# Performance work log

Hardware: AMD Instinct MI355X
Metric: run time of the kernel (lower is better)

## Reference

```python
import jax, jax.numpy as jnp
import numpy as np


def setup_inputs() -> dict:
    key = jax.random.key(0)
    k1, k2, k3, k4, k5 = jax.random.split(key, 5)
    N, V, C = 4096, 4, 256
    desc = jax.random.normal(k1, (N, V, C), dtype=jnp.float32)
    sf = jax.random.normal(k2, (N, V, C), dtype=jnp.float32)
    T = jax.random.normal(k3, (V, 4, 4), dtype=jnp.float32)
    W_rec = jax.random.normal(k4, (C, C), dtype=jnp.float32) * (1.0 / np.sqrt(C))
    W_T = jax.random.normal(k5, (32, C), dtype=jnp.float32) * (1.0 / np.sqrt(32))
    return {"desc": desc, "sf": sf, "T": T, "W_rec": W_rec, "W_T": W_T}


def reference(desc, sf, T, W_rec, W_T):
    # desc, sf: [N, V, C]; T: [V, 4, 4]
    N, V, C = desc.shape
    # F.normalize(desc, dim=2)
    dn = desc / jnp.maximum(jnp.linalg.norm(desc, axis=2, keepdims=True), 1e-12)
    ar = jnp.arange(N)
    loss_total = jnp.zeros((), dtype=desc.dtype)
    count = jnp.zeros((), dtype=desc.dtype)
    for i in range(V):
        for j in range(V):
            if i == j:
                continue
            di = dn[:, i, :]  # [N, C]
            dj = dn[:, j, :]  # [N, C]
            sim = di @ dj.T   # [N, N]
            idx_ij = jnp.argmax(sim, axis=1)
            idx_ji = jnp.argmax(sim, axis=0)
            mutual = (idx_ji[idx_ij] == ar)  # [N] bool, mutual nearest neighbors
            # kpnet.reconstruction(desc_i, T_i, T_j): linear, transform-conditioned
            rel = jnp.concatenate([T[i].ravel(), T[j].ravel()])  # [32]
            sf_recon = di @ W_rec + rel @ W_T  # [N, C]
            # torch.no_grad() block -> stop_gradient
            prob = jax.nn.softmax(sim, axis=1)
            sf_j_soft = jax.lax.stop_gradient(prob @ sf[:, j, :])  # [N, C]
            m = mutual.astype(desc.dtype)[:, None]  # [N, 1]
            n_sel = jnp.sum(m)
            sq = jnp.sum(((sf_recon - sf_j_soft) ** 2) * m)
            pair_loss = sq / jnp.maximum(n_sel * C, 1.0)  # masked MSE (mean over selected elems)
            valid = (n_sel > 0).astype(desc.dtype)
            loss_total = loss_total + valid * pair_loss
            count = count + valid
    return jnp.where(count > 0, loss_total / jnp.maximum(count, 1.0), 0.0 * jnp.sum(desc))
```

## Files before the change

kernel.cpp:

```cpp
#include <hip/hip_runtime.h>
#include <math.h>

#define N_ 4096
#define V_ 4
#define C_ 256

typedef __attribute__((ext_vector_type(8))) short bf16x8;
typedef __attribute__((ext_vector_type(4))) float f32x4;
typedef unsigned long long u64;

#define OFF_R      0ull
#define OFF_DNHI   16777216ull
#define OFF_DNLO   25165824ull
#define OFF_SFT    33554432ull
#define OFF_E      37748736ull
#define OFF_ET     88080384ull
#define OFF_WTH    138412032ull
#define OFF_WTL    138543104ull
#define OFF_ROWPK  138674176ull
#define OFF_COLPK  138870784ull
#define OFF_ROWSM  139067392ull
#define OFF_COLSM  139165696ull
#define OFF_RELWT  139264000ull
#define OFF_SQ     139280384ull
#define OFF_CNT    139280448ull

__device__ __forceinline__ unsigned short f2bf(float x) {
    unsigned int u = __float_as_uint(x);
    u += 0x7fffu + ((u >> 16) & 1u);
    return (unsigned short)(u >> 16);
}
__device__ __forceinline__ float bf2f(unsigned short h) {
    return __uint_as_float(((unsigned int)h) << 16);
}
__device__ __forceinline__ f32x4 mfma16(bf16x8 a, bf16x8 b, f32x4 c) {
    return __builtin_amdgcn_mfma_f32_16x16x32_bf16(a, b, c, 0, 0, 0);
}
__device__ __forceinline__ unsigned int pk4fp8(float x0, float x1, float x2, float x3) {
    int w = 0;
    w = __builtin_amdgcn_cvt_pk_fp8_f32(x0, x1, w, false);
    w = __builtin_amdgcn_cvt_pk_fp8_f32(x2, x3, w, true);
    return (unsigned int)w;
}

__global__ void normalize_k(const float* __restrict__ desc,
                            unsigned short* __restrict__ dnh, unsigned short* __restrict__ dnl) {
    int row = blockIdx.x;
    int n = row >> 2, v = row & 3;
    int c = threadIdx.x;
    float x = desc[(size_t)row * C_ + c];
    __shared__ float red[256];
    red[c] = x * x;
    __syncthreads();
    for (int s = 128; s > 0; s >>= 1) {
        if (c < s) red[c] += red[c + s];
        __syncthreads();
    }
    float inv = 1.0f / fmaxf(sqrtf(red[0]), 1e-12f);
    float y = x * inv;
    size_t o = ((size_t)v * N_ + n) * C_ + c;
    unsigned short h = f2bf(y);
    dnh[o] = h;
    dnl[o] = f2bf(y - bf2f(h));
}

__global__ void wrecT_k(const float* __restrict__ W, unsigned short* __restrict__ WTh,
                        unsigned short* __restrict__ WTl) {
    __shared__ float Tt[64 * 65];
    int k0 = blockIdx.x * 64, c0 = blockIdx.y * 64;
    int t = threadIdx.x;
    int kr = t >> 2, cq = (t & 3) * 16;
    const float* src = W + (size_t)(k0 + kr) * C_ + c0 + cq;
    for (int u = 0; u < 16; ++u) Tt[(cq + u) * 65 + kr] = src[u];
    __syncthreads();
    int cr = t >> 2, kq = (t & 3) * 16;
    unsigned short th[16] __attribute__((aligned(16)));
    unsigned short tl[16] __attribute__((aligned(16)));
    for (int u = 0; u < 16; ++u) {
        float x = Tt[cr * 65 + kq + u];
        unsigned short h = f2bf(x);
        th[u] = h; tl[u] = f2bf(x - bf2f(h));
    }
    size_t o = (size_t)(c0 + cr) * C_ + k0 + kq;
    *(uint4*)(WTh + o) = *(const uint4*)th;
    *(uint4*)(WTh + o + 8) = *(const uint4*)(th + 8);
    *(uint4*)(WTl + o) = *(const uint4*)tl;
    *(uint4*)(WTl + o + 8) = *(const uint4*)(tl + 8);
}

__global__ __launch_bounds__(256) void rmatmul_k(
    const unsigned short* __restrict__ Ah, const unsigned short* __restrict__ Al,
    const unsigned short* __restrict__ Bh, const unsigned short* __restrict__ Bl,
    float* __restrict__ R) {
    __shared__ unsigned short smem[4 * 128 * 40];
    unsigned short* sAh = smem;
    unsigned short* sAl = sAh + 128 * 40;
    unsigned short* sBh = sAl + 128 * 40;
    unsigned short* sBl = sBh + 128 * 40;
    int tid = threadIdx.x;
    int c0 = blockIdx.x * 128, m0 = blockIdx.y * 128;
    int w = tid >> 6, l = tid & 63, wm = w & 1, wn = w >> 1;
    int mr = l & 15, q = l >> 4;
    f32x4 acc[4][4];
#pragma unroll
    for (int a = 0; a < 4; ++a)
#pragma unroll
        for (int b = 0; b < 4; ++b)
#pragma unroll
            for (int u = 0; u < 4; ++u) acc[a][b][u] = 0.f;
    int r = tid >> 1, h = (tid & 1) * 16;
    for (int k0 = 0; k0 < C_; k0 += 32) {
        size_t ga = (size_t)(m0 + r) * C_ + k0 + h;
        size_t gb = (size_t)(c0 + r) * C_ + k0 + h;
        uint4 a0 = *(const uint4*)(Ah + ga);
        uint4 a1 = *(const uint4*)(Ah + ga + 8);
        uint4 a2 = *(const uint4*)(Al + ga);
        uint4 a3 = *(const uint4*)(Al + ga + 8);
        uint4 b0 = *(const uint4*)(Bh + gb);
        uint4 b1 = *(const uint4*)(Bh + gb + 8);
        uint4 b2 = *(const uint4*)(Bl + gb);
        uint4 b3 = *(const uint4*)(Bl + gb + 8);
        *(uint4*)(sAh + r * 40 + h)     = a0;
        *(uint4*)(sAh + r * 40 + h + 8) = a1;
        *(uint4*)(sAl + r * 40 + h)     = a2;
        *(uint4*)(sAl + r * 40 + h + 8) = a3;
        *(uint4*)(sBh + r * 40 + h)     = b0;
        *(uint4*)(sBh + r * 40 + h + 8) = b1;
        *(uint4*)(sBl + r * 40 + h)     = b2;
        *(uint4*)(sBl + r * 40 + h + 8) = b3;
        __syncthreads();
        bf16x8 fah[4], fal[4], fbh[4], fbl[4];
#pragma unroll
        for (int ti = 0; ti < 4; ++ti) {
            int row = wm * 64 + ti * 16 + mr;
            fah[ti] = *(const bf16x8*)(sAh + row * 40 + q * 8);
            fal[ti] = *(const bf16x8*)(sAl + row * 40 + q * 8);
        }
#pragma unroll
        for (int tj = 0; tj < 4; ++tj) {
            int row = wn * 64 + tj * 16 + mr;
            fbh[tj] = *(const bf16x8*)(sBh + row * 40 + q * 8);
            fbl[tj] = *(const bf16x8*)(sBl + row * 40 + q * 8);
        }
#pragma unroll
        for (int ti = 0; ti < 4; ++ti)
#pragma unroll
            for (int tj = 0; tj < 4; ++tj) acc[ti][tj] = mfma16(fah[ti], fbh[tj], acc[ti][tj]);
#pragma unroll
        for (int ti = 0; ti < 4; ++ti)
#pragma unroll
            for (int tj = 0; tj < 4; ++tj) acc[ti][tj] = mfma16(fah[ti], fbl[tj], acc[ti][tj]);
#pragma unroll
        for (int ti = 0; ti < 4; ++ti)
#pragma unroll
            for (int tj = 0; tj < 4; ++tj) acc[ti][tj] = mfma16(fal[ti], fbh[tj], acc[ti][tj]);
        __syncthreads();
    }
#pragma unroll
    for (int ti = 0; ti < 4; ++ti)
#pragma unroll
        for (int tj = 0; tj < 4; ++tj) {
            int c = c0 + wn * 64 + tj * 16 + mr;
#pragma unroll
            for (int rg = 0; rg < 4; ++rg) {
                int m = m0 + wm * 64 + ti * 16 + q * 4 + rg;
                R[(size_t)m * C_ + c] = acc[ti][tj][rg];
            }
        }
}

__global__ void relwt_k(const float* __restrict__ T, const float* __restrict__ WT,
                        float* __restrict__ relwt) {
    int p = blockIdx.x; int i = p >> 2, j = p & 3;
    if (i == j) return;
    int c = threadIdx.x;
    float acc = 0.f;
    for (int k = 0; k < 16; ++k) acc += T[i * 16 + k] * WT[(size_t)k * C_ + c];
    for (int k = 0; k < 16; ++k) acc += T[j * 16 + k] * WT[(size_t)(16 + k) * C_ + c];
    relwt[(size_t)p * C_ + c] = acc;
}

__global__ void sfT_k(const float* __restrict__ sf, unsigned char* __restrict__ sf8T) {
    __shared__ float Tt[64 * 65];
    int n0 = blockIdx.x * 64, c0 = blockIdx.y * 64, v = blockIdx.z;
    int t = threadIdx.x;
    int nr = t >> 2, cq = (t & 3) * 16;
    const float* src = sf + ((size_t)(n0 + nr) * V_ + v) * C_ + c0 + cq;
    for (int u = 0; u < 16; ++u) Tt[(cq + u) * 65 + nr] = src[u];
    __syncthreads();
    int cr = t >> 2, nq = (t & 3) * 16;
    unsigned int wb[4];
#pragma unroll
    for (int g = 0; g < 4; ++g) {
        const float* p = Tt + cr * 65 + nq + g * 4;
        wb[g] = pk4fp8(p[0], p[1], p[2], p[3]);
    }
    unsigned char* dst = sf8T + ((size_t)v * C_ + c0 + cr) * N_ + n0 + nq;
    *(uint4*)dst = make_uint4(wb[0], wb[1], wb[2], wb[3]);
}

__global__ void zero_k(u64* rowPk, u64* colPk, float* rowSm, float* colSm,
                       float* sq, int* cnt) {
    int idx = blockIdx.x * 256 + threadIdx.x;
    rowPk[idx] = 0ull; colPk[idx] = 0ull;
    rowSm[idx] = 0.f;  colSm[idx] = 0.f;
    if (idx < 16) { sq[idx] = 0.f; cnt[idx] = 0; }
}

__global__ __launch_bounds__(256) void sim_mfma_k(
    const unsigned short* __restrict__ dnh, const unsigned short* __restrict__ dnl,
    int ipack, int jpack, unsigned char* __restrict__ E8b, unsigned char* __restrict__ ET8b,
    u64* __restrict__ rowPkB, float* __restrict__ rowSmB,
    u64* __restrict__ colPkB, float* __restrict__ colSmB, int slotBase) {
    __shared__ unsigned char smem[36864];
    __shared__ float sRedM[256];
    __shared__ int   sRedA[256];
    __shared__ float sRedS[256];
    unsigned short* sAh = (unsigned short*)smem;
    unsigned short* sAl = sAh + 64 * 72;
    unsigned short* sBh = sAl + 64 * 72;
    unsigned short* sBl = sBh + 64 * 72;
    float* S = (float*)smem;

    int zp = blockIdx.z;
    int iv = (ipack >> (8 * zp)) & 15;
    int jv = (jpack >> (8 * zp)) & 15;
    const unsigned short* Ahi = dnh + (size_t)iv * N_ * C_;
    const unsigned short* Alo = dnl + (size_t)iv * N_ * C_;
    const unsigned short* Bhi = dnh + (size_t)jv * N_ * C_;
    const unsigned short* Blo = dnl + (size_t)jv * N_ * C_;
    unsigned char* E8  = E8b  + (size_t)zp * N_ * N_;
    unsigned char* ET8 = ET8b + (size_t)zp * N_ * N_;
    int slot = slotBase + zp;
    u64*   rowPk = rowPkB + (size_t)slot * N_;
    float* rowSm = rowSmB + (size_t)slot * N_;
    u64*   colPk = colPkB + (size_t)slot * N_;
    float* colSm = colSmB + (size_t)slot * N_;

    int tid = threadIdx.x;
    int m0 = blockIdx.y * 64, n0 = blockIdx.x * 64;
    int w = tid >> 6, l = tid & 63;
    int wm = w & 1, wn = w >> 1;
    int mr = l & 15, q = l >> 4;

    f32x4 acc[2][2];
#pragma unroll
    for (int a = 0; a < 2; ++a)
#pragma unroll
        for (int b = 0; b < 2; ++b)
#pragma unroll
            for (int u = 0; u < 4; ++u) acc[a][b][u] = 0.f;

    int r = tid >> 2;
    int k8 = (tid & 3) * 8;
    const unsigned short* gAh = Ahi + (size_t)(m0 + r) * C_ + k8;
    const unsigned short* gAl = Alo + (size_t)(m0 + r) * C_ + k8;
    const unsigned short* gBh = Bhi + (size_t)(n0 + r) * C_ + k8;
    const unsigned short* gBl = Blo + (size_t)(n0 + r) * C_ + k8;

    uint4 a0 = *(const uint4*)(gAh);
    uint4 a1 = *(const uint4*)(gAh + 32);
    uint4 a2 = *(const uint4*)(gAl);
    uint4 a3 = *(const uint4*)(gAl + 32);
    uint4 b0 = *(const uint4*)(gBh);
    uint4 b1 = *(const uint4*)(gBh + 32);
    uint4 b2 = *(const uint4*)(gBl);
    uint4 b3 = *(const uint4*)(gBl + 32);

    for (int k0 = 0; k0 < C_; k0 += 64) {
        *(uint4*)(sAh + r * 72 + k8)      = a0;
        *(uint4*)(sAh + r * 72 + k8 + 32) = a1;
        *(uint4*)(sAl + r * 72 + k8)      = a2;
        *(uint4*)(sAl + r * 72 + k8 + 32) = a3;
        *(uint4*)(sBh + r * 72 + k8)      = b0;
        *(uint4*)(sBh + r * 72 + k8 + 32) = b1;
        *(uint4*)(sBl + r * 72 + k8)      = b2;
        *(uint4*)(sBl + r * 72 + k8 + 32) = b3;
        __syncthreads();
        int kn = k0 + 64;
        if (kn < C_) {
            a0 = *(const uint4*)(gAh + kn);
            a1 = *(const uint4*)(gAh + kn + 32);
            a2 = *(const uint4*)(gAl + kn);
            a3 = *(const uint4*)(gAl + kn + 32);
            b0 = *(const uint4*)(gBh + kn);
            b1 = *(const uint4*)(gBh + kn + 32);
            b2 = *(const uint4*)(gBl + kn);
            b3 = *(const uint4*)(gBl + kn + 32);
        }
#pragma unroll
        for (int ks = 0; ks < 64; ks += 32) {
            bf16x8 ah[2], al[2], bh[2], bl[2];
#pragma unroll
            for (int ti = 0; ti < 2; ++ti) {
                int mrow = wm * 32 + ti * 16 + mr;
                ah[ti] = *(const bf16x8*)(sAh + mrow * 72 + ks + q * 8);
                al[ti] = *(const bf16x8*)(sAl + mrow * 72 + ks + q * 8);
            }
#pragma unroll
            for (int tj = 0; tj < 2; ++tj) {
                int nrow = wn * 32 + tj * 16 + mr;
                bh[tj] = *(const bf16x8*)(sBh + nrow * 72 + ks + q * 8);
                bl[tj] = *(const bf16x8*)(sBl + nrow * 72 + ks + q * 8);
            }
#pragma unroll
            for (int ti = 0; ti < 2; ++ti)
#pragma unroll
                for (int tj = 0; tj < 2; ++tj) {
                    acc[ti][tj] = mfma16(ah[ti], bh[tj], acc[ti][tj]);
                    acc[ti][tj] = mfma16(ah[ti], bl[tj], acc[ti][tj]);
                    acc[ti][tj] = mfma16(al[ti], bh[tj], acc[ti][tj]);
                }
        }
        __syncthreads();
    }

#pragma unroll
    for (int ti = 0; ti < 2; ++ti)
#pragma unroll
        for (int tj = 0; tj < 2; ++tj)
#pragma unroll
            for (int rg = 0; rg < 4; ++rg)
                S[(wm * 32 + ti * 16 + q * 4 + rg) * 65 + wn * 32 + tj * 16 + mr] =
                    __expf(acc[ti][tj][rg]);
    __syncthreads();

    {
        int rr = tid >> 2, q4 = tid & 3;
        float mx = -1e30f; int ag = 0; float sm = 0.f;
        for (int cc = 0; cc < 16; ++cc) {
            int c = q4 * 16 + cc;
            float v = S[rr * 65 + c];
            sm += v;
            if (v > mx) { mx = v; ag = c; }
        }
        sRedM[tid] = mx; sRedA[tid] = ag; sRedS[tid] = sm;
    }
    __syncthreads();
    if (tid < 64) {
        float mx = -1e30f; int ag = 0; float sm = 0.f;
        for (int qq = 0; qq < 4; ++qq) {
            float v = sRedM[tid * 4 + qq];
            if (v > mx) { mx = v; ag = sRedA[tid * 4 + qq]; }
            sm += sRedS[tid * 4 + qq];
        }
        u64 pk = ((u64)__float_as_uint(mx) << 32) | (u64)(0xFFFFFFFFu - (unsigned)(n0 + ag));
        atomicMax(rowPk + m0 + tid, pk);
        atomicAdd(rowSm + m0 + tid, sm);
    }
    __syncthreads();
    {
        int cc = tid >> 2, q4 = tid & 3;
        float mx = -1e30f; int ag = 0; float sm = 0.f;
        for (int rr = 0; rr < 16; ++rr) {
            int rrr = q4 * 16 + rr;
            float v = S[rrr * 65 + cc];
            sm += v;
            if (v > mx) { mx = v; ag = rrr; }
        }
        sRedM[tid] = mx; sRedA[tid] = ag; sRedS[tid] = sm;
    }
    __syncthreads();
    if (tid < 64) {
        float mx = -1e30f; int ag = 0; float sm = 0.f;
        for (int qq = 0; qq < 4; ++qq) {
            float v = sRedM[tid * 4 + qq];
            if (v > mx) { mx = v; ag = sRedA[tid * 4 + qq]; }
            sm += sRedS[tid * 4 + qq];
        }
        u64 pk = ((u64)__float_as_uint(mx) << 32) | (u64)(0xFFFFFFFFu - (unsigned)(m0 + ag));
        atomicMax(colPk + n0 + tid, pk);
        atomicAdd(colSm + n0 + tid, sm);
    }
    {
        int r2 = tid >> 2, cq = (tid & 3) * 16;
        unsigned int wb[4];
#pragma unroll
        for (int g = 0; g < 4; ++g) {
            const float* p = S + r2 * 65 + cq + g * 4;
            wb[g] = pk4fp8(p[0], p[1], p[2], p[3]);
        }
        *(uint4*)(E8 + (size_t)(m0 + r2) * N_ + n0 + cq) = make_uint4(wb[0], wb[1], wb[2], wb[3]);
    }
    {
        int n2 = tid >> 2, mq = (tid & 3) * 16;
        unsigned int wb[4];
#pragma unroll
        for (int g = 0; g < 4; ++g) {
            wb[g] = pk4fp8(S[(mq + g * 4 + 0) * 65 + n2], S[(mq + g * 4 + 1) * 65 + n2],
                           S[(mq + g * 4 + 2) * 65 + n2], S[(mq + g * 4 + 3) * 65 + n2]);
        }
        *(uint4*)(ET8 + (size_t)(n0 + n2) * N_ + m0 + mq) = make_uint4(wb[0], wb[1], wb[2], wb[3]);
    }
}

__global__ __launch_bounds__(256) void p2_k(
    const unsigned char* __restrict__ E8b, const unsigned char* __restrict__ ET8b,
    const unsigned char* __restrict__ sf8T, int ipack, int jpack,
    const u64* __restrict__ rowPkB, const float* __restrict__ rowSmB,
    const u64* __restrict__ colPkB, const float* __restrict__ colSmB, int slotBase,
    const float* __restrict__ R, const float* __restrict__ relwt,
    float* __restrict__ pairSq, int* __restrict__ pairCnt) {
    __shared__ unsigned char sA[64 * 80];
    __shared__ unsigned char sB[128 * 80];
    __shared__ float red[256];
    __shared__ int   mutS[64];
    __shared__ float invS[64];
    int tid = threadIdx.x;
    int ct = blockIdx.x & 1, mt = blockIdx.x >> 1;
    int d = blockIdx.y & 1, zp = blockIdx.y >> 1;
    int iv = (ipack >> (8 * zp)) & 15;
    int jv = (jpack >> (8 * zp)) & 15;
    int slot = slotBase + zp;
    const unsigned char* A = (d ? ET8b : E8b) + (size_t)zp * N_ * N_;
    const unsigned char* B = sf8T + (size_t)(d ? iv : jv) * C_ * N_;
    const u64* faPk = (d ? colPkB : rowPkB) + (size_t)slot * N_;
    const u64* baPk = (d ? rowPkB : colPkB) + (size_t)slot * N_;
    const float* sumE = (d ? colSmB : rowSmB) + (size_t)slot * N_;
    const float* Rr = R + (size_t)(d ? jv : iv) * N_ * C_;
    int pid = d ? (jv * 4 + iv) : (iv * 4 + jv);
    int c0 = ct * 128, m0 = mt * 64;
    int w = tid >> 6, l = tid & 63, wm = w & 1, wn = w >> 1;
    int mr = l & 15, q = l >> 4;
    if (tid < 64) {
        int y = m0 + tid;
        unsigned faIdx = 0xFFFFFFFFu - (unsigned)(faPk[y] & 0xFFFFFFFFull);
        unsigned baIdx = 0xFFFFFFFFu - (unsigned)(baPk[faIdx] & 0xFFFFFFFFull);
        mutS[tid] = (baIdx == (unsigned)y) ? 1 : 0;
        invS[tid] = 1.0f / sumE[y];
    }
    f32x4 acc[2][4];
#pragma unroll
    for (int a = 0; a < 2; ++a)
#pragma unroll
        for (int b = 0; b < 4; ++b)
#pragma unroll
            for (int u = 0; u < 4; ++u) acc[a][b][u] = 0.f;

    int ra = tid >> 2, ka = (tid & 3) * 16;
    int rb = tid >> 1, kbb = (tid & 1) * 32;
    const unsigned char* Arow = A + (size_t)(m0 + ra) * N_ + ka;
    const unsigned char* Brow = B + (size_t)(c0 + rb) * N_ + kbb;
    uint4 pa  = *(const uint4*)(Arow);
    uint4 pb0 = *(const uint4*)(Brow);
    uint4 pb1 = *(const uint4*)(Brow + 16);
    for (int k0 = 0; k0 < N_; k0 += 64) {
        *(uint4*)(sA + ra * 80 + ka)       = pa;
        *(uint4*)(sB + rb * 80 + kbb)      = pb0;
        *(uint4*)(sB + rb * 80 + kbb + 16) = pb1;
        __syncthreads();
        int kn = k0 + 64;
        if (kn < N_) {
            pa  = *(const uint4*)(Arow + kn);
            pb0 = *(const uint4*)(Brow + kn);
            pb1 = *(const uint4*)(Brow + kn + 16);
        }
#pragma unroll
        for (int ksub = 0; ksub < 64; ksub += 32) {
            long af[2], bf[4];
#pragma unroll
            for (int ti = 0; ti < 2; ++ti)
                af[ti] = *(const long*)(sA + (wm * 32 + ti * 16 + mr) * 80 + ksub + q * 8);
#pragma unroll
            for (int tj = 0; tj < 4; ++tj)
                bf[tj] = *(const long*)(sB + (wn * 64 + tj * 16 + mr) * 80 + ksub + q * 8);
#pragma unroll
            for (int ti = 0; ti < 2; ++ti)
#pragma unroll
                for (int tj = 0; tj < 4; ++tj)
                    acc[ti][tj] = __builtin_amdgcn_mfma_f32_16x16x32_fp8_fp8(
                        af[ti], bf[tj], acc[ti][tj], 0, 0, 0);
        }
        __syncthreads();
    }
    const float* rw = relwt + (size_t)pid * C_;
    float local = 0.f;
#pragma unroll
    for (int ti = 0; ti < 2; ++ti)
#pragma unroll
        for (int tj = 0; tj < 4; ++tj) {
            int c = c0 + wn * 64 + tj * 16 + mr;
            float rwc = rw[c];
#pragma unroll
            for (int rg = 0; rg < 4; ++rg) {
                int ml = wm * 32 + ti * 16 + q * 4 + rg;
                if (mutS[ml]) {
                    int m = m0 + ml;
                    float soft = acc[ti][tj][rg] * invS[ml];
                    float dv = Rr[(size_t)m * C_ + c] + rwc - soft;
                    local += dv * dv;
                }
            }
        }
    red[tid] = local;
    __syncthreads();
    for (int s = 128; s > 0; s >>= 1) {
        if (tid < s) red[tid] += red[tid + s];
        __syncthreads();
    }
    if (tid == 0) {
        atomicAdd(pairSq + pid, red[0]);
        if (ct == 0) {
            int cnt = 0;
            for (int u = 0; u < 64; ++u) cnt += mutS[u];
            atomicAdd(pairCnt + pid, cnt);
        }
    }
}

__global__ void final_k(const float* __restrict__ sq, const int* __restrict__ cnt,
                        float* __restrict__ out) {
    if (threadIdx.x == 0 && blockIdx.x == 0) {
        float loss = 0.f, count = 0.f;
        for (int p = 0; p < 16; ++p) {
            int i = p >> 2, j = p & 3;
            if (i == j) continue;
            float ns = (float)cnt[p];
            if (ns > 0.f) { loss += sq[p] / fmaxf(ns * (float)C_, 1.0f); count += 1.f; }
        }
        out[0] = (count > 0.f) ? loss / count : 0.f;
    }
}

extern "C" void kernel_launch(void* const* d_in, const int* in_sizes, int n_in,
                              void* d_out, int out_size, void* d_ws, size_t ws_size,
                              hipStream_t stream) {
    const float* desc = (const float*)d_in[0];
    const float* sf   = (const float*)d_in[1];
    const float* T    = (const float*)d_in[2];
    const float* Wrec = (const float*)d_in[3];
    const float* WT   = (const float*)d_in[4];
    float* out = (float*)d_out;
    char* ws = (char*)d_ws;

    float*          R     = (float*)(ws + OFF_R);
    unsigned short* dnh   = (unsigned short*)(ws + OFF_DNHI);
    unsigned short* dnl   = (unsigned short*)(ws + OFF_DNLO);
    unsigned char*  sf8T  = (unsigned char*)(ws + OFF_SFT);
    unsigned char*  E8b   = (unsigned char*)(ws + OFF_E);
    unsigned char*  ET8b  = (unsigned char*)(ws + OFF_ET);
    unsigned short* WTh   = (unsigned short*)(ws + OFF_WTH);
    unsigned short* WTl   = (unsigned short*)(ws + OFF_WTL);
    u64*   rowPk = (u64*)(ws + OFF_ROWPK);
    u64*   colPk = (u64*)(ws + OFF_COLPK);
    float* rowSm = (float*)(ws + OFF_ROWSM);
    float* colSm = (float*)(ws + OFF_COLSM);
    float* relwt = (float*)(ws + OFF_RELWT);
    float* pairSq = (float*)(ws + OFF_SQ);
    int*   pairCnt = (int*)(ws + OFF_CNT);

    normalize_k<<<N_ * V_, 256, 0, stream>>>(desc, dnh, dnl);
    wrecT_k<<<dim3(4, 4), 256, 0, stream>>>(Wrec, WTh, WTl);
    rmatmul_k<<<dim3(2, 128), 256, 0, stream>>>(dnh, dnl, WTh, WTl, R);
    sfT_k<<<dim3(64, 4, 4), 256, 0, stream>>>(sf, sf8T);
    relwt_k<<<16, 256, 0, stream>>>(T, WT, relwt);
    zero_k<<<96, 256, 0, stream>>>(rowPk, colPk, rowSm, colSm, pairSq, pairCnt);

    const int ip[2] = { 0 | (0 << 8) | (0 << 16), 1 | (1 << 8) | (2 << 16) };
    const int jp[2] = { 1 | (2 << 8) | (3 << 16), 2 | (3 << 8) | (3 << 16) };
    for (int b = 0; b < 2; ++b) {
        sim_mfma_k<<<dim3(64, 64, 3), 256, 0, stream>>>(
            dnh, dnl, ip[b], jp[b], E8b, ET8b, rowPk, rowSm, colPk, colSm, b * 3);
        p2_k<<<dim3(128, 6), 256, 0, stream>>>(
            E8b, ET8b, sf8T, ip[b], jp[b], rowPk, rowSm, colPk, colSm, b * 3,
            R, relwt, pairSq, pairCnt);
    }
    final_k<<<1, 64, 0, stream>>>(pairSq, pairCnt, out);
}
```

Before: 508.0 us.

## Enlarge sim tile to 128x128 with LDS DMA double-buffering and shuffle reductions

Raises the similarity GEMM tile from 64x64 to 128x128 so each block does more MFMA work per load. Operands are fetched with global_load_lds DMA into double-buffered, XOR-swizzled LDS, replacing the register-staged copies. The row and column argmax reductions now run in registers with wave shuffles, and the exp tile is staged in LDS as bf16 to fit the larger tile. The bf16 staging slightly changes the stored values and the sums, and the larger accumulator array raises register pressure.

```diff
diff --git a/kernel.cpp b/kernel.cpp
--- a/kernel.cpp
+++ b/kernel.cpp
@@ -41,6 +41,15 @@
     w = __builtin_amdgcn_cvt_pk_fp8_f32(x0, x1, w, false);
     w = __builtin_amdgcn_cvt_pk_fp8_f32(x2, x3, w, true);
     return (unsigned int)w;
+}
+__device__ __forceinline__ u64 max64(u64 a, u64 b) { return a > b ? a : b; }
+__device__ __forceinline__ u64 packkey(float v, int idx) {
+    return ((u64)__float_as_uint(v) << 32) | (u64)(0xFFFFFFFFu - (unsigned)idx);
+}
+__device__ __forceinline__ void dma16(const void* g, void* l) {
+    __builtin_amdgcn_global_load_lds(
+        (const __attribute__((address_space(1))) unsigned int*)g,
+        (__attribute__((address_space(3))) unsigned int*)l, 16, 0, 0);
 }
 
 __global__ void normalize_k(const float* __restrict__ desc,
@@ -207,28 +216,31 @@
     if (idx < 16) { sq[idx] = 0.f; cnt[idx] = 0; }
 }
 
-__global__ __launch_bounds__(256) void sim_mfma_k(
+__device__ __forceinline__ void dma_stage(const unsigned short* A_h, const unsigned short* A_l,
+                                          const unsigned short* B_h, const unsigned short* B_l,
+                                          char* lbase, int w, int laneOff, int k0) {
+#pragma unroll
+    for (int gg = 0; gg < 2; ++gg) {
+        int g = w * 2 + gg;
+        size_t go = (size_t)g * 16 * C_ + k0 + laneOff;
+        char* lb = lbase + g * 1024;
+        dma16(A_h + go, lb);
+        dma16(A_l + go, lb + 8192);
+        dma16(B_h + go, lb + 16384);
+        dma16(B_l + go, lb + 24576);
+    }
+}
+
+__global__ __launch_bounds__(256, 2) void sim_mfma_k(
     const unsigned short* __restrict__ dnh, const unsigned short* __restrict__ dnl,
     int ipack, int jpack, unsigned char* __restrict__ E8b, unsigned char* __restrict__ ET8b,
     u64* __restrict__ rowPkB, float* __restrict__ rowSmB,
     u64* __restrict__ colPkB, float* __restrict__ colSmB, int slotBase) {
-    __shared__ unsigned char smem[36864];
-    __shared__ float sRedM[256];
-    __shared__ int   sRedA[256];
-    __shared__ float sRedS[256];
-    unsigned short* sAh = (unsigned short*)smem;
-    unsigned short* sAl = sAh + 64 * 72;
-    unsigned short* sBh = sAl + 64 * 72;
-    unsigned short* sBl = sBh + 64 * 72;
-    float* S = (float*)smem;
+    __shared__ char smem[65536];
 
     int zp = blockIdx.z;
     int iv = (ipack >> (8 * zp)) & 15;
     int jv = (jpack >> (8 * zp)) & 15;
-    const unsigned short* Ahi = dnh + (size_t)iv * N_ * C_;
-    const unsigned short* Alo = dnl + (size_t)iv * N_ * C_;
-    const unsigned short* Bhi = dnh + (size_t)jv * N_ * C_;
-    const unsigned short* Blo = dnl + (size_t)jv * N_ * C_;
     unsigned char* E8  = E8b  + (size_t)zp * N_ * N_;
     unsigned char* ET8 = ET8b + (size_t)zp * N_ * N_;
     int slot = slotBase + zp;
@@ -238,159 +250,153 @@
     float* colSm = colSmB + (size_t)slot * N_;
 
     int tid = threadIdx.x;
-    int m0 = blockIdx.y * 64, n0 = blockIdx.x * 64;
+    int n0 = blockIdx.x * 128, m0 = blockIdx.y * 128;
     int w = tid >> 6, l = tid & 63;
     int wm = w & 1, wn = w >> 1;
     int mr = l & 15, q = l >> 4;
-
-    f32x4 acc[2][2];
-#pragma unroll
-    for (int a = 0; a < 2; ++a)
-#pragma unroll
-        for (int b = 0; b < 2; ++b)
+    int sl = q ^ ((mr >> 1) & 3);
+
+    int rowoff = l >> 2;
+    int laneOff = rowoff * C_ + (((l & 3) ^ ((rowoff >> 1) & 3)) * 8);
+
+    const unsigned short* Ah0 = dnh + (size_t)iv * N_ * C_ + (size_t)m0 * C_;
+    const unsigned short* Al0 = dnl + (size_t)iv * N_ * C_ + (size_t)m0 * C_;
+    const unsigned short* Bh0 = dnh + (size_t)jv * N_ * C_ + (size_t)n0 * C_;
+    const unsigned short* Bl0 = dnl + (size_t)jv * N_ * C_ + (size_t)n0 * C_;
+
+    f32x4 acc[4][4];
+#pragma unroll
+    for (int a = 0; a < 4; ++a)
+#pragma unroll
+        for (int b = 0; b < 4; ++b)
 #pragma unroll
             for (int u = 0; u < 4; ++u) acc[a][b][u] = 0.f;
 
-    int r = tid >> 2;
-    int k8 = (tid & 3) * 8;
-    const unsigned short* gAh = Ahi + (size_t)(m0 + r) * C_ + k8;
-    const unsigned short* gAl = Alo + (size_t)(m0 + r) * C_ + k8;
-    const unsigned short* gBh = Bhi + (size_t)(n0 + r) * C_ + k8;
-    const unsigned short* gBl = Blo + (size_t)(n0 + r) * C_ + k8;
-
-    uint4 a0 = *(const uint4*)(gAh);
-    uint4 a1 = *(const uint4*)(gAh + 32);
-    uint4 a2 = *(const uint4*)(gAl);
-    uint4 a3 = *(const uint4*)(gAl + 32);
-    uint4 b0 = *(const uint4*)(gBh);
-    uint4 b1 = *(const uint4*)(gBh + 32);
-    uint4 b2 = *(const uint4*)(gBl);
-    uint4 b3 = *(const uint4*)(gBl + 32);
-
-    for (int k0 = 0; k0 < C_; k0 += 64) {
-        *(uint4*)(sAh + r * 72 + k8)      = a0;
-        *(uint4*)(sAh + r * 72 + k8 + 32) = a1;
-        *(uint4*)(sAl + r * 72 + k8)      = a2;
-        *(uint4*)(sAl + r * 72 + k8 + 32) = a3;
-        *(uint4*)(sBh + r * 72 + k8)      = b0;
-        *(uint4*)(sBh + r * 72 + k8 + 32) = b1;
-        *(uint4*)(sBl + r * 72 + k8)      = b2;
-        *(uint4*)(sBl + r * 72 + k8 + 32) = b3;
-        __syncthreads();
-        int kn = k0 + 64;
-        if (kn < C_) {
-            a0 = *(const uint4*)(gAh + kn);
-            a1 = *(const uint4*)(gAh + kn + 32);
-            a2 = *(const uint4*)(gAl + kn);
-            a3 = *(const uint4*)(gAl + kn + 32);
-            b0 = *(const uint4*)(gBh + kn);
-            b1 = *(const uint4*)(gBh + kn + 32);
-            b2 = *(const uint4*)(gBl + kn);
-            b3 = *(const uint4*)(gBl + kn + 32);
-        }
-#pragma unroll
-        for (int ks = 0; ks < 64; ks += 32) {
-            bf16x8 ah[2], al[2], bh[2], bl[2];
-#pragma unroll
-            for (int ti = 0; ti < 2; ++ti) {
-                int mrow = wm * 32 + ti * 16 + mr;
-                ah[ti] = *(const bf16x8*)(sAh + mrow * 72 + ks + q * 8);
-                al[ti] = *(const bf16x8*)(sAl + mrow * 72 + ks + q * 8);
+    dma_stage(Ah0, Al0, Bh0, Bl0, smem, w, laneOff, 0);
+    int buf = 0;
+#pragma unroll 2
+    for (int kc = 0; kc < 8; ++kc) {
+        if (kc < 7) {
+            dma_stage(Ah0, Al0, Bh0, Bl0, smem + (buf ^ 1) * 32768, w, laneOff, (kc + 1) * 32);
+            asm volatile("s_waitcnt vmcnt(8)" ::: "memory");
+        } else {
+            asm volatile("s_waitcnt vmcnt(0)" ::: "memory");
+        }
+        __builtin_amdgcn_s_barrier();
+        __builtin_amdgcn_sched_barrier(0);
+        const unsigned short* sb = (const unsigned short*)(smem + buf * 32768);
+        bf16x8 ah[4], al[4], bh[4], bl[4];
+#pragma unroll
+        for (int ti = 0; ti < 4; ++ti) {
+            int row = wm * 64 + ti * 16 + mr;
+            ah[ti] = *(const bf16x8*)(sb + row * 32 + sl * 8);
+            al[ti] = *(const bf16x8*)(sb + 4096 + row * 32 + sl * 8);
+        }
+#pragma unroll
+        for (int tj = 0; tj < 4; ++tj) {
+            int row = wn * 64 + tj * 16 + mr;
+            bh[tj] = *(const bf16x8*)(sb + 8192 + row * 32 + sl * 8);
+            bl[tj] = *(const bf16x8*)(sb + 12288 + row * 32 + sl * 8);
+        }
+#pragma unroll
+        for (int ti = 0; ti < 4; ++ti)
+#pragma unroll
+            for (int tj = 0; tj < 4; ++tj) {
+                acc[ti][tj] = mfma16(ah[ti], bh[tj], acc[ti][tj]);
+                acc[ti][tj] = mfma16(ah[ti], bl[tj], acc[ti][tj]);
+                acc[ti][tj] = mfma16(al[ti], bh[tj], acc[ti][tj]);
             }
-#pragma unroll
-            for (int tj = 0; tj < 2; ++tj) {
-                int nrow = wn * 32 + tj * 16 + mr;
-                bh[tj] = *(const bf16x8*)(sBh + nrow * 72 + ks + q * 8);
-                bl[tj] = *(const bf16x8*)(sBl + nrow * 72 + ks + q * 8);
+        __builtin_amdgcn_sched_barrier(0);
+        __builtin_amdgcn_s_barrier();
+        __builtin_amdgcn_sched_barrier(0);
+        buf ^= 1;
+    }
+
+#pragma unroll
+    for (int ti = 0; ti < 4; ++ti)
+#pragma unroll
+        for (int tj = 0; tj < 4; ++tj)
+#pragma unroll
+            for (int rg = 0; rg < 4; ++rg)
+                acc[ti][tj][rg] = __expf(acc[ti][tj][rg]);
+
+    unsigned short* S16 = (unsigned short*)smem;
+#pragma unroll
+    for (int ti = 0; ti < 4; ++ti)
+#pragma unroll
+        for (int tj = 0; tj < 4; ++tj)
+#pragma unroll
+            for (int rg = 0; rg < 4; ++rg)
+                S16[(wm * 64 + ti * 16 + q * 4 + rg) * 132 + wn * 64 + tj * 16 + mr] =
+                    f2bf(acc[ti][tj][rg]);
+
+#pragma unroll
+    for (int ti = 0; ti < 4; ++ti)
+#pragma unroll
+        for (int rg = 0; rg < 4; ++rg) {
+            u64 best = 0ull;
+#pragma unroll
+            for (int tj = 0; tj < 4; ++tj)
+                best = max64(best, packkey(acc[ti][tj][rg], n0 + wn * 64 + tj * 16 + mr));
+            best = max64(best, __shfl_xor(best, 1));
+            best = max64(best, __shfl_xor(best, 2));
+            best = max64(best, __shfl_xor(best, 4));
+            best = max64(best, __shfl_xor(best, 8));
+            if (mr == 0) atomicMax(rowPk + m0 + wm * 64 + ti * 16 + q * 4 + rg, best);
+        }
+#pragma unroll
+    for (int tj = 0; tj < 4; ++tj) {
+        u64 best = 0ull;
+#pragma unroll
+        for (int ti = 0; ti < 4; ++ti)
+#pragma unroll
+            for (int rg = 0; rg < 4; ++rg)
+                best = max64(best, packkey(acc[ti][tj][rg], m0 + wm * 64 + ti * 16 + q * 4 + rg));
+        best = max64(best, __shfl_xor(best, 16));
+        best = max64(best, __shfl_xor(best, 32));
+        if (q == 0) atomicMax(colPk + n0 + wn * 64 + tj * 16 + mr, best);
+    }
+    __syncthreads();
+
+    {
+        int rr = tid & 127, hf = tid >> 7;
+        const unsigned short* Sr = S16 + rr * 132 + hf * 64;
+        unsigned char* dst = E8 + (size_t)(m0 + rr) * N_ + n0 + hf * 64;
+        float sum = 0.f;
+#pragma unroll
+        for (int g = 0; g < 4; ++g) {
+            unsigned int wb[4];
+#pragma unroll
+            for (int h2 = 0; h2 < 4; ++h2) {
+                ushort4 vv = *(const ushort4*)(Sr + g * 16 + h2 * 4);
+                float f0 = bf2f(vv.x), f1 = bf2f(vv.y), f2 = bf2f(vv.z), f3 = bf2f(vv.w);
+                sum += (f0 + f1) + (f2 + f3);
+                wb[h2] = pk4fp8(f0, f1, f2, f3);
             }
-#pragma unroll
-            for (int ti = 0; ti < 2; ++ti)
-#pragma unroll
-                for (int tj = 0; tj < 2; ++tj) {
-                    acc[ti][tj] = mfma16(ah[ti], bh[tj], acc[ti][tj]);
-                    acc[ti][tj] = mfma16(ah[ti], bl[tj], acc[ti][tj]);
-                    acc[ti][tj] = mfma16(al[ti], bh[tj], acc[ti][tj]);
-                }
-        }
-        __syncthreads();
-    }
-
-#pragma unroll
-    for (int ti = 0; ti < 2; ++ti)
-#pragma unroll
-        for (int tj = 0; tj < 2; ++tj)
-#pragma unroll
-            for (int rg = 0; rg < 4; ++rg)
-                S[(wm * 32 + ti * 16 + q * 4 + rg) * 65 + wn * 32 + tj * 16 + mr] =
-                    __expf(acc[ti][tj][rg]);
-    __syncthreads();
-
+            *(uint4*)(dst + g * 16) = make_uint4(wb[0], wb[1], wb[2], wb[3]);
+        }
+        atomicAdd(rowSm + m0 + rr, sum);
+    }
     {
-        int rr = tid >> 2, q4 = tid & 3;
-        float mx = -1e30f; int ag = 0; float sm = 0.f;
-        for (int cc = 0; cc < 16; ++cc) {
-            int c = q4 * 16 + cc;
-            float v = S[rr * 65 + c];
-            sm += v;
-            if (v > mx) { mx = v; ag = c; }
-        }
-        sRedM[tid] = mx; sRedA[tid] = ag; sRedS[tid] = sm;
-    }
-    __syncthreads();
-    if (tid < 64) {
-        float mx = -1e30f; int ag = 0; float sm = 0.f;
-        for (int qq = 0; qq < 4; ++qq) {
-            float v = sRedM[tid * 4 + qq];
-            if (v > mx) { mx = v; ag = sRedA[tid * 4 + qq]; }
-            sm += sRedS[tid * 4 + qq];
-        }
-        u64 pk = ((u64)__float_as_uint(mx) << 32) | (u64)(0xFFFFFFFFu - (unsigned)(n0 + ag));
-        atomicMax(rowPk + m0 + tid, pk);
-        atomicAdd(rowSm + m0 + tid, sm);
-    }
-    __syncthreads();
-    {
-        int cc = tid >> 2, q4 = tid & 3;
-        float mx = -1e30f; int ag = 0; float sm = 0.f;
-        for (int rr = 0; rr < 16; ++rr) {
-            int rrr = q4 * 16 + rr;
-            float v = S[rrr * 65 + cc];
-            sm += v;
-            if (v > mx) { mx = v; ag = rrr; }
-        }
-        sRedM[tid] = mx; sRedA[tid] = ag; sRedS[tid] = sm;
-    }
-    __syncthreads();
-    if (tid < 64) {
-        float mx = -1e30f; int ag = 0; float sm = 0.f;
-        for (int qq = 0; qq < 4; ++qq) {
-            float v = sRedM[tid * 4 + qq];
-            if (v > mx) { mx = v; ag = sRedA[tid * 4 + qq]; }
-            sm += sRedS[tid * 4 + qq];
-        }
-        u64 pk = ((u64)__float_as_uint(mx) << 32) | (u64)(0xFFFFFFFFu - (unsigned)(m0 + ag));
-        atomicMax(colPk + n0 + tid, pk);
-        atomicAdd(colSm + n0 + tid, sm);
-    }
-    {
-        int r2 = tid >> 2, cq = (tid & 3) * 16;
-        unsigned int wb[4];
+        int cc = tid & 127, hf = tid >> 7;
+        unsigned char* dst = ET8 + (size_t)(n0 + cc) * N_ + m0 + hf * 64;
+        float sum = 0.f;
 #pragma unroll
         for (int g = 0; g < 4; ++g) {
-            const float* p = S + r2 * 65 + cq + g * 4;
-            wb[g] = pk4fp8(p[0], p[1], p[2], p[3]);
-        }
-        *(uint4*)(E8 + (size_t)(m0 + r2) * N_ + n0 + cq) = make_uint4(wb[0], wb[1], wb[2], wb[3]);
-    }
-    {
-        int n2 = tid >> 2, mq = (tid & 3) * 16;
-        unsigned int wb[4];
-#pragma unroll
-        for (int g = 0; g < 4; ++g) {
-            wb[g] = pk4fp8(S[(mq + g * 4 + 0) * 65 + n2], S[(mq + g * 4 + 1) * 65 + n2],
-                           S[(mq + g * 4 + 2) * 65 + n2], S[(mq + g * 4 + 3) * 65 + n2]);
-        }
-        *(uint4*)(ET8 + (size_t)(n0 + n2) * N_ + m0 + mq) = make_uint4(wb[0], wb[1], wb[2], wb[3]);
+            unsigned int wb[4];
+#pragma unroll
+            for (int h2 = 0; h2 < 4; ++h2) {
+                int rb = hf * 64 + g * 16 + h2 * 4;
+                float f0 = bf2f(S16[(rb + 0) * 132 + cc]);
+                float f1 = bf2f(S16[(rb + 1) * 132 + cc]);
+                float f2 = bf2f(S16[(rb + 2) * 132 + cc]);
+                float f3 = bf2f(S16[(rb + 3) * 132 + cc]);
+                sum += (f0 + f1) + (f2 + f3);
+                wb[h2] = pk4fp8(f0, f1, f2, f3);
+            }
+            *(uint4*)(dst + g * 16) = make_uint4(wb[0], wb[1], wb[2], wb[3]);
+        }
+        atomicAdd(colSm + n0 + cc, sum);
     }
 }
 
@@ -559,7 +565,7 @@
     const int ip[2] = { 0 | (0 << 8) | (0 << 16), 1 | (1 << 8) | (2 << 16) };
     const int jp[2] = { 1 | (2 << 8) | (3 << 16), 2 | (3 << 8) | (3 << 16) };
     for (int b = 0; b < 2; ++b) {
-        sim_mfma_k<<<dim3(64, 64, 3), 256, 0, stream>>>(
+        sim_mfma_k<<<dim3(32, 32, 3), 256, 0, stream>>>(
             dnh, dnl, ip[b], jp[b], E8b, ET8b, rowPk, rowSm, colPk, colSm, b * 3);
         p2_k<<<dim3(128, 6), 256, 0, stream>>>(
             E8b, ET8b, sf8T, ip[b], jp[b], rowPk, rowSm, colPk, colSm, b * 3,
```

New measurement: 558.3 us. 1.1x slower.
